# Kernel optimization log

Measured on AMD Instinct MI355X. Metric: run time of the kernel, lower is better.

The kernel has to match this reference:

```python
import jax, jax.numpy as jnp
import numpy as np

D_MODEL, N_HEADS, D_VALUE = 512, 8, 64
D_HEAD = D_MODEL // N_HEADS


def setup_inputs() -> dict:
    key = jax.random.key(0)
    ks = jax.random.split(key, 5)
    B, T = 2, 2048
    x = jax.random.normal(ks[0], (B, T, D_MODEL), dtype=jnp.float32)
    # torch nn.Linear convention: W has shape [out_features, in_features]
    scale = 0.02
    W_q = jax.random.normal(ks[1], (N_HEADS * D_HEAD, D_MODEL), dtype=jnp.float32) * scale
    W_k = jax.random.normal(ks[2], (N_HEADS * D_HEAD, D_MODEL), dtype=jnp.float32) * scale
    W_v = jax.random.normal(ks[3], (N_HEADS * D_VALUE, D_MODEL), dtype=jnp.float32) * scale
    W_out = jax.random.normal(ks[4], (D_MODEL, N_HEADS * D_VALUE), dtype=jnp.float32) * scale
    return {"x": x, "W_q": W_q, "W_k": W_k, "W_v": W_v, "W_out": W_out}


def _elu_feature_map(t):
    # phi(t) = elu(t) + 1
    return jax.nn.elu(t) + 1.0


def reference(x, W_q, W_k, W_v, W_out):
    B, T, D = x.shape
    H, dh, dv = N_HEADS, D_HEAD, D_VALUE
    # projections (Linear without bias: x @ W.T)
    Q = _elu_feature_map((x @ W_q.T).reshape(B, T, H, dh)).transpose(0, 2, 1, 3)  # [B,H,T,dh]
    K = _elu_feature_map((x @ W_k.T).reshape(B, T, H, dh)).transpose(0, 2, 1, 3)  # [B,H,T,dh]
    V = (x @ W_v.T).reshape(B, T, H, dv).transpose(0, 2, 1, 3)                    # [B,H,T,dv]
    # causal linear attention via cumulative outer-product state
    KV = jnp.einsum('bhti,bhtj->bhtij', K, V)       # [B,H,T,dh,dv]
    S = jnp.cumsum(KV, axis=2)                      # running state
    z = jnp.cumsum(K, axis=2)                       # running normalizer
    num = jnp.einsum('bhti,bhtij->bhtj', Q, S)      # [B,H,T,dv]
    den = jnp.maximum(jnp.einsum('bhti,bhti->bht', Q, z), 1e-6)[..., None]
    out = (num / den).transpose(0, 2, 1, 3).reshape(B, T, H * dv)
    return out @ W_out.T
```

## Files before the change

kernel.cpp:

```cpp
#include <hip/hip_runtime.h>
#include <hip/hip_bf16.h>

#define T_SEQ 2048
#define BATCH 2
#define DMODEL 512
#define NHEAD 8
#define DHEAD 64
#define DVAL 64
#define BH 16
#define CHUNK 64
#define NCHUNK 32
#define MROWS 4096

typedef __bf16 bf16;
typedef __bf16 bf16x8 __attribute__((ext_vector_type(8)));
typedef __bf16 bf16x4 __attribute__((ext_vector_type(4)));
typedef float f32x4 __attribute__((ext_vector_type(4)));

__device__ inline void gload_lds16(const bf16* g, bf16* l) {
  __builtin_amdgcn_global_load_lds((const __attribute__((address_space(1))) void*)g,
                                   (__attribute__((address_space(3))) void*)l, 16, 0, 0);
}

__device__ inline int sw_t(int row, int g) {
  return ((g ^ (row & 7) ^ (row >> 3)) << 3);
}

__global__ __launch_bounds__(256) void k_convert(const float* __restrict__ x,
                          const float* __restrict__ wq,
                          const float* __restrict__ wk,
                          const float* __restrict__ wv,
                          const float* __restrict__ wo,
                          bf16* __restrict__ x_bf,
                          bf16* __restrict__ wqkv_bf,
                          bf16* __restrict__ wo_bf) {
  const int W = DMODEL * DMODEL;
  int i = blockIdx.x * 256 + threadIdx.x;
  {
    f32x4 v = ((const f32x4*)x)[i];
    bf16x4 o; o[0] = (bf16)v[0]; o[1] = (bf16)v[1]; o[2] = (bf16)v[2]; o[3] = (bf16)v[3];
    *(bf16x4*)(x_bf + (size_t)i * 4) = o;
  }
  if (i < W / 4) {
    f32x4 a = ((const f32x4*)wq)[i];
    f32x4 b = ((const f32x4*)wk)[i];
    f32x4 c = ((const f32x4*)wv)[i];
    f32x4 d = ((const f32x4*)wo)[i];
    bf16x4 oa, ob, oc, od;
#pragma unroll
    for (int u = 0; u < 4; u++) { oa[u] = (bf16)a[u]; ob[u] = (bf16)b[u]; oc[u] = (bf16)c[u]; od[u] = (bf16)d[u]; }
    *(bf16x4*)(wqkv_bf + (size_t)i * 4) = oa;
    *(bf16x4*)(wqkv_bf + W + (size_t)i * 4) = ob;
    *(bf16x4*)(wqkv_bf + 2 * W + (size_t)i * 4) = oc;
    *(bf16x4*)(wo_bf + (size_t)i * 4) = od;
  }
}

template <int EPI>
__global__ __launch_bounds__(256) void k_gemm(const bf16* __restrict__ A,
                                              const bf16* __restrict__ B,
                                              bf16* __restrict__ Q,
                                              bf16* __restrict__ K,
                                              bf16* __restrict__ V,
                                              float* __restrict__ out) {
  __shared__ bf16 As[128 * 64];
  __shared__ bf16 Bs[128 * 64];
  const int tid = threadIdx.x;
  const int wv = tid >> 6, lane = tid & 63;
  const int c = lane & 15, quad = lane >> 4;
  const int m_tile = blockIdx.x * 128, n_tile = blockIdx.y * 128;
  const int r8 = lane >> 3, gp = lane & 7;
  const bf16* Abase = A + (size_t)m_tile * DMODEL;
  const bf16* Bbase = B + (size_t)n_tile * DMODEL;
  const int wm = (wv >> 1) * 64, wn = (wv & 1) * 64;

  f32x4 acc[4][4] = {};

  for (int k0 = 0; k0 < DMODEL; k0 += 64) {
    if (k0) __syncthreads();
#pragma unroll
    for (int r = 0; r < 4; r++) {
      int t = wv * 4 + r;
      const bf16* ga = Abase + (size_t)(t * 8 + r8) * DMODEL + k0 + ((gp ^ r8) << 3);
      const bf16* gb = Bbase + (size_t)(t * 8 + r8) * DMODEL + k0 + ((gp ^ r8) << 3);
      gload_lds16(ga, As + t * 8 * 64);
      gload_lds16(gb, Bs + t * 8 * 64);
    }
    __syncthreads();
#pragma unroll
    for (int ks = 0; ks < 2; ks++) {
      bf16x8 af[4], bfr[4];
#pragma unroll
      for (int i = 0; i < 4; i++)
        af[i] = *(const bf16x8*)(As + (wm + i * 16 + c) * 64 + (((ks * 4 + quad) ^ (c & 7)) << 3));
#pragma unroll
      for (int j = 0; j < 4; j++)
        bfr[j] = *(const bf16x8*)(Bs + (wn + j * 16 + c) * 64 + (((ks * 4 + quad) ^ (c & 7)) << 3));
#pragma unroll
      for (int i = 0; i < 4; i++)
#pragma unroll
        for (int j = 0; j < 4; j++)
          acc[i][j] = __builtin_amdgcn_mfma_f32_16x16x32_bf16(af[i], bfr[j], acc[i][j], 0, 0, 0);
    }
  }

#pragma unroll
  for (int i = 0; i < 4; i++) {
#pragma unroll
    for (int j = 0; j < 4; j++) {
      int n = n_tile + wn + j * 16 + c;
#pragma unroll
      for (int r = 0; r < 4; r++) {
        int m = m_tile + wm + i * 16 + quad * 4 + r;
        float v = acc[i][j][r];
        if (EPI == 0) {
          if (n < 1024) v = (v > 0.f) ? (v + 1.f) : __expf(v);
          bf16 o = (bf16)v;
          if (n < 512)       Q[(size_t)m * 512 + n] = o;
          else if (n < 1024) K[(size_t)m * 512 + (n - 512)] = o;
          else               V[(size_t)m * 512 + (n - 1024)] = o;
        } else {
          out[(size_t)m * DMODEL + n] = v;
        }
      }
    }
  }
}

__global__ __launch_bounds__(256) void k_state(const bf16* __restrict__ K,
                                               const bf16* __restrict__ V,
                                               bf16* __restrict__ KVs,
                                               float* __restrict__ zsum) {
  __shared__ bf16 Kt[4096];
  __shared__ bf16 Vt[4096];
  int chunk = blockIdx.x, bh = blockIdx.y;
  int b = bh >> 3, h = bh & 7;
  int tid = threadIdx.x, lane = tid & 63, wv = tid >> 6;
  int rowbase = b * T_SEQ + chunk * CHUNK;

#pragma unroll
  for (int p = 0; p < 2; p++) {
    int r = p * 32 + (tid >> 3);
    int j0 = (tid & 7) * 8;
    bf16x8 kk = *(const bf16x8*)(K + (size_t)(rowbase + r) * 512 + h * 64 + j0);
    bf16x8 vvv = *(const bf16x8*)(V + (size_t)(rowbase + r) * 512 + h * 64 + j0);
#pragma unroll
    for (int u = 0; u < 8; u++) {
      int row = j0 + u;
      Kt[row * 64 + sw_t(row, r >> 3) + (r & 7)] = kk[u];
      Vt[row * 64 + sw_t(row, r >> 3) + (r & 7)] = vvv[u];
    }
  }
  __syncthreads();

  int c = lane & 15, quad = lane >> 4;
  f32x4 acc[4] = {};
#pragma unroll
  for (int ks = 0; ks < 2; ks++) {
    int ar = wv * 16 + c;
    bf16x8 a = *(const bf16x8*)(Vt + ar * 64 + sw_t(ar, ks * 4 + quad));
#pragma unroll
    for (int f = 0; f < 4; f++) {
      int br = f * 16 + c;
      bf16x8 bb = *(const bf16x8*)(Kt + br * 64 + sw_t(br, ks * 4 + quad));
      acc[f] = __builtin_amdgcn_mfma_f32_16x16x32_bf16(a, bb, acc[f], 0, 0, 0);
    }
  }
  bf16* op = KVs + ((size_t)(bh * NCHUNK + chunk) << 12);
#pragma unroll
  for (int f = 0; f < 4; f++)
#pragma unroll
    for (int r = 0; r < 4; r++)
      op[(wv * 16 + quad * 4 + r) * 64 + f * 16 + c] = (bf16)acc[f][r];

  if (tid < 64) {
    float s = 0.f;
#pragma unroll
    for (int g = 0; g < 8; g++) {
      bf16x8 kr = *(const bf16x8*)(Kt + tid * 64 + sw_t(tid, g));
#pragma unroll
      for (int u = 0; u < 8; u++) s += (float)kr[u];
    }
    zsum[(size_t)(bh * NCHUNK + chunk) * 64 + tid] = s;
  }
}

__global__ __launch_bounds__(256) void k_attn(const bf16* __restrict__ Q,
                                              const bf16* __restrict__ K,
                                              const bf16* __restrict__ V,
                                              const bf16* __restrict__ KVs,
                                              const float* __restrict__ zsum,
                                              bf16* __restrict__ O) {
  __shared__ bf16 Qs[4096];
  __shared__ bf16 Ks[4096];
  __shared__ bf16 Vt[4096];
  __shared__ bf16 As[4096];
  __shared__ bf16 Spre[4096];
  __shared__ float zp4[4][64];
  __shared__ float zpre[64], rsum[64], den[64];

  int chunk = blockIdx.x, bh = blockIdx.y;
  int b = bh >> 3, h = bh & 7;
  int tid = threadIdx.x, lane = tid & 63, wv = tid >> 6;
  int c = lane & 15, quad = lane >> 4;
  int rowbase = b * T_SEQ + chunk * CHUNK;

#pragma unroll
  for (int p = 0; p < 2; p++) {
    int rbase = p * 32 + wv * 8;
    int r8 = lane >> 3, gp = lane & 7;
    const bf16* gq = Q + (size_t)(rowbase + rbase + r8) * 512 + h * 64 + ((gp ^ r8) << 3);
    const bf16* gk = K + (size_t)(rowbase + rbase + r8) * 512 + h * 64 + ((gp ^ r8) << 3);
    gload_lds16(gq, Qs + rbase * 64);
    gload_lds16(gk, Ks + rbase * 64);
  }

#pragma unroll
  for (int p = 0; p < 2; p++) {
    int r = p * 32 + (tid >> 3);
    int j0 = (tid & 7) * 8;
    bf16x8 vvv = *(const bf16x8*)(V + (size_t)(rowbase + r) * 512 + h * 64 + j0);
#pragma unroll
    for (int u = 0; u < 8; u++) {
      int row = j0 + u;
      Vt[row * 64 + sw_t(row, r >> 3) + (r & 7)] = vvv[u];
    }
  }

  {
    float accp[16];
#pragma unroll
    for (int u = 0; u < 16; u++) accp[u] = 0.f;
    const bf16* base = KVs + ((size_t)(bh * NCHUNK) << 12) + tid * 16;
    for (int cc = 0; cc < chunk; cc++) {
      const bf16* pp = base + ((size_t)cc << 12);
      bf16x8 a0 = *(const bf16x8*)pp;
      bf16x8 a1 = *(const bf16x8*)(pp + 8);
#pragma unroll
      for (int u = 0; u < 8; u++) { accp[u] += (float)a0[u]; accp[8 + u] += (float)a1[u]; }
    }
    int j = tid >> 2, i0 = (tid & 3) * 16;
#pragma unroll
    for (int u = 0; u < 16; u++) {
      int i = i0 + u;
      Spre[j * 64 + sw_t(j, i >> 3) + (i & 7)] = (bf16)accp[u];
    }
  }

  {
    int i = tid & 63, qq = tid >> 6;
    float s = 0.f;
    for (int cc = qq; cc < chunk; cc += 4)
      s += zsum[(size_t)(bh * NCHUNK + cc) * 64 + i];
    zp4[qq][i] = s;
  }
  __syncthreads();
  if (tid < 64) zpre[tid] = zp4[0][tid] + zp4[1][tid] + zp4[2][tid] + zp4[3][tid];

  f32x4 sacc[4] = {};
#pragma unroll
  for (int ks = 0; ks < 2; ks++) {
    int ar = 16 * wv + c;
    bf16x8 a = *(const bf16x8*)(Qs + ar * 64 + (((ks * 4 + quad) ^ (c & 7)) << 3));
#pragma unroll
    for (int j = 0; j < 4; j++) {
      int br = 16 * j + c;
      bf16x8 bb = *(const bf16x8*)(Ks + br * 64 + (((ks * 4 + quad) ^ (c & 7)) << 3));
      sacc[j] = __builtin_amdgcn_mfma_f32_16x16x32_bf16(a, bb, sacc[j], 0, 0, 0);
    }
  }

  float rs[4] = {0.f, 0.f, 0.f, 0.f};
#pragma unroll
  for (int j = 0; j < 4; j++) {
#pragma unroll
    for (int r = 0; r < 4; r++) {
      int t = 16 * wv + quad * 4 + r, s = 16 * j + c;
      float v = (s <= t) ? sacc[j][r] : 0.f;
      rs[r] += v;
      As[t * 64 + sw_t(t, s >> 3) + (s & 7)] = (bf16)v;
    }
  }
#pragma unroll
  for (int r = 0; r < 4; r++) {
    float v = rs[r];
    v += __shfl_xor(v, 1); v += __shfl_xor(v, 2);
    v += __shfl_xor(v, 4); v += __shfl_xor(v, 8);
    if (c == 0) rsum[16 * wv + quad * 4 + r] = v;
  }
  __syncthreads();

  if (tid < 64) {
    float s = rsum[tid];
    int t7 = tid & 7;
#pragma unroll
    for (int kg = 0; kg < 8; kg++) {
      bf16x8 qv = *(const bf16x8*)(Qs + tid * 64 + ((kg ^ t7) << 3));
#pragma unroll
      for (int u = 0; u < 8; u++) s += (float)qv[u] * zpre[kg * 8 + u];
    }
    den[tid] = fmaxf(s, 1e-6f);
  }

  f32x4 oacc[4] = {};
#pragma unroll
  for (int ks = 0; ks < 2; ks++) {
    int ar = 16 * wv + c;
    bf16x8 aq = *(const bf16x8*)(Qs + ar * 64 + (((ks * 4 + quad) ^ (c & 7)) << 3));
    bf16x8 aa = *(const bf16x8*)(As + ar * 64 + sw_t(ar, ks * 4 + quad));
#pragma unroll
    for (int j = 0; j < 4; j++) {
      int br = 16 * j + c;
      bf16x8 bs = *(const bf16x8*)(Spre + br * 64 + sw_t(br, ks * 4 + quad));
      bf16x8 bv = *(const bf16x8*)(Vt + br * 64 + sw_t(br, ks * 4 + quad));
      oacc[j] = __builtin_amdgcn_mfma_f32_16x16x32_bf16(aq, bs, oacc[j], 0, 0, 0);
      oacc[j] = __builtin_amdgcn_mfma_f32_16x16x32_bf16(aa, bv, oacc[j], 0, 0, 0);
    }
  }
  __syncthreads();
#pragma unroll
  for (int r = 0; r < 4; r++) {
    int t = 16 * wv + quad * 4 + r;
    float rd = 1.f / den[t];
#pragma unroll
    for (int j = 0; j < 4; j++)
      O[(size_t)(rowbase + t) * 512 + h * 64 + 16 * j + c] = (bf16)(oacc[j][r] * rd);
  }
}

extern "C" void kernel_launch(void* const* d_in, const int* in_sizes, int n_in,
                              void* d_out, int out_size, void* d_ws, size_t ws_size,
                              hipStream_t stream) {
  const float* x  = (const float*)d_in[0];
  const float* wq = (const float*)d_in[1];
  const float* wk = (const float*)d_in[2];
  const float* wv = (const float*)d_in[3];
  const float* wo = (const float*)d_in[4];
  float* out = (float*)d_out;

  char* p = (char*)d_ws;
  bf16* x_bf   = (bf16*)p; p += (size_t)MROWS * DMODEL * 2;
  bf16* wqkv_b = (bf16*)p; p += (size_t)3 * DMODEL * DMODEL * 2;
  bf16* wo_b   = (bf16*)p; p += (size_t)DMODEL * DMODEL * 2;
  bf16* Qb     = (bf16*)p; p += (size_t)MROWS * 512 * 2;
  bf16* Kb     = (bf16*)p; p += (size_t)MROWS * 512 * 2;
  bf16* Vb     = (bf16*)p; p += (size_t)MROWS * 512 * 2;
  bf16* Ob     = (bf16*)p; p += (size_t)MROWS * 512 * 2;
  bf16* KVs    = (bf16*)p; p += (size_t)BH * NCHUNK * DHEAD * DVAL * 2;
  float* zs    = (float*)p; p += (size_t)BH * NCHUNK * DHEAD * 4;

  k_convert<<<2048, 256, 0, stream>>>(x, wq, wk, wv, wo, x_bf, wqkv_b, wo_b);
  k_gemm<0><<<dim3(MROWS / 128, (3 * DMODEL) / 128), 256, 0, stream>>>(
      x_bf, wqkv_b, Qb, Kb, Vb, nullptr);
  k_state<<<dim3(NCHUNK, BH), 256, 0, stream>>>(Kb, Vb, KVs, zs);
  k_attn<<<dim3(NCHUNK, BH), 256, 0, stream>>>(Qb, Kb, Vb, KVs, zs, Ob);
  k_gemm<1><<<dim3(MROWS / 128, DMODEL / 128), 256, 0, stream>>>(
      Ob, wo_b, nullptr, nullptr, nullptr, out);
}
```

Measured before the change: 119.9 us.

## Fuse chunk-state and attention kernels via cooperative grid sync; stage GEMM epilogues through LDS

Merges the per-chunk KV state kernel into the attention kernel and joins them with a cooperative grid-wide sync, so K and V are loaded once and one launch is removed. The GEMM epilogues now stage tiles through shared memory so the Q/K/V and output writes go out as coalesced 16-byte vectors, and the attention output is written the same way. The per-chunk state is stored in a fragment-native layout, and the prefix-sum read path is changed to match. A grid sync over 512 blocks needs every block to be resident at once. It also adds sync latency and more shared memory per block.

```diff
diff --git a/kernel.cpp b/kernel.cpp
--- a/kernel.cpp
+++ b/kernel.cpp
@@ -1,5 +1,6 @@
 #include <hip/hip_runtime.h>
 #include <hip/hip_bf16.h>
+#include <hip/hip_cooperative_groups.h>
 
 #define T_SEQ 2048
 #define BATCH 2
@@ -63,16 +64,17 @@
                                               bf16* __restrict__ K,
                                               bf16* __restrict__ V,
                                               float* __restrict__ out) {
-  __shared__ bf16 As[128 * 64];
-  __shared__ bf16 Bs[128 * 64];
+  __shared__ bf16 sh[16896];
+  bf16* As = sh;
+  bf16* Bs = sh + 8192;
   const int tid = threadIdx.x;
-  const int wv = tid >> 6, lane = tid & 63;
+  const int wvi = tid >> 6, lane = tid & 63;
   const int c = lane & 15, quad = lane >> 4;
   const int m_tile = blockIdx.x * 128, n_tile = blockIdx.y * 128;
   const int r8 = lane >> 3, gp = lane & 7;
   const bf16* Abase = A + (size_t)m_tile * DMODEL;
   const bf16* Bbase = B + (size_t)n_tile * DMODEL;
-  const int wm = (wv >> 1) * 64, wn = (wv & 1) * 64;
+  const int wm = (wvi >> 1) * 64, wn = (wvi & 1) * 64;
 
   f32x4 acc[4][4] = {};
 
@@ -80,7 +82,7 @@
     if (k0) __syncthreads();
 #pragma unroll
     for (int r = 0; r < 4; r++) {
-      int t = wv * 4 + r;
+      int t = wvi * 4 + r;
       const bf16* ga = Abase + (size_t)(t * 8 + r8) * DMODEL + k0 + ((gp ^ r8) << 3);
       const bf16* gb = Bbase + (size_t)(t * 8 + r8) * DMODEL + k0 + ((gp ^ r8) << 3);
       gload_lds16(ga, As + t * 8 * 64);
@@ -104,110 +106,81 @@
     }
   }
 
-#pragma unroll
-  for (int i = 0; i < 4; i++) {
-#pragma unroll
-    for (int j = 0; j < 4; j++) {
-      int n = n_tile + wn + j * 16 + c;
-#pragma unroll
-      for (int r = 0; r < 4; r++) {
-        int m = m_tile + wm + i * 16 + quad * 4 + r;
-        float v = acc[i][j][r];
-        if (EPI == 0) {
-          if (n < 1024) v = (v > 0.f) ? (v + 1.f) : __expf(v);
-          bf16 o = (bf16)v;
-          if (n < 512)       Q[(size_t)m * 512 + n] = o;
-          else if (n < 1024) K[(size_t)m * 512 + (n - 512)] = o;
-          else               V[(size_t)m * 512 + (n - 1024)] = o;
-        } else {
-          out[(size_t)m * DMODEL + n] = v;
+  if (EPI == 0) {
+    const bool is_qk = (n_tile < 1024);
+    __syncthreads();
+#pragma unroll
+    for (int i = 0; i < 4; i++)
+#pragma unroll
+      for (int j = 0; j < 4; j++)
+#pragma unroll
+        for (int r = 0; r < 4; r++) {
+          int row = wm + i * 16 + quad * 4 + r;
+          int col = wn + j * 16 + c;
+          float v = acc[i][j][r];
+          if (is_qk) v = (v > 0.f) ? (v + 1.f) : __expf(v);
+          sh[row * 132 + col] = (bf16)v;
         }
+    __syncthreads();
+    bf16* dst = (n_tile < 512) ? Q : ((n_tile < 1024) ? K : V);
+    int nb = n_tile & 511;
+#pragma unroll
+    for (int q = 0; q < 8; q++) {
+      int row = q * 16 + (tid >> 4);
+      int col0 = (tid & 15) * 8;
+      bf16x8 v8 = *(const bf16x8*)(sh + row * 132 + col0);
+      *(bf16x8*)(dst + (size_t)(m_tile + row) * 512 + nb + col0) = v8;
+    }
+  } else {
+    float* shf = (float*)sh;
+#pragma unroll
+    for (int p = 0; p < 2; p++) {
+      __syncthreads();
+      if ((wvi >> 1) == p) {
+#pragma unroll
+        for (int i = 0; i < 4; i++)
+#pragma unroll
+          for (int j = 0; j < 4; j++)
+#pragma unroll
+            for (int r = 0; r < 4; r++)
+              shf[(i * 16 + quad * 4 + r) * 132 + wn + j * 16 + c] = acc[i][j][r];
       }
-    }
-  }
-}
-
-__global__ __launch_bounds__(256) void k_state(const bf16* __restrict__ K,
-                                               const bf16* __restrict__ V,
-                                               bf16* __restrict__ KVs,
-                                               float* __restrict__ zsum) {
-  __shared__ bf16 Kt[4096];
-  __shared__ bf16 Vt[4096];
+      __syncthreads();
+      int row = tid >> 2, col0 = (tid & 3) * 32;
+#pragma unroll
+      for (int q4 = 0; q4 < 8; q4++) {
+        f32x4 v4 = *(const f32x4*)(shf + row * 132 + col0 + q4 * 4);
+        *(f32x4*)(out + (size_t)(m_tile + p * 64 + row) * 512 + n_tile + col0 + q4 * 4) = v4;
+      }
+    }
+  }
+}
+
+__global__ __launch_bounds__(256) void k_attn_fused(const bf16* __restrict__ Q,
+                                                    const bf16* __restrict__ K,
+                                                    const bf16* __restrict__ V,
+                                                    bf16* __restrict__ KVs,
+                                                    float* __restrict__ zsum,
+                                                    bf16* __restrict__ O) {
+  __shared__ bf16 SH[24576];
+  bf16* Qs   = SH;
+  bf16* Ks   = SH + 4096;
+  bf16* Vt   = SH + 8192;
+  bf16* Kt   = SH + 12288;
+  bf16* Asm  = SH + 16384;
+  bf16* Spre = SH + 20480;
+  __shared__ float zp4[4][64];
+  __shared__ float zpre[64], rsum[64], den[64];
+
   int chunk = blockIdx.x, bh = blockIdx.y;
   int b = bh >> 3, h = bh & 7;
-  int tid = threadIdx.x, lane = tid & 63, wv = tid >> 6;
-  int rowbase = b * T_SEQ + chunk * CHUNK;
-
-#pragma unroll
-  for (int p = 0; p < 2; p++) {
-    int r = p * 32 + (tid >> 3);
-    int j0 = (tid & 7) * 8;
-    bf16x8 kk = *(const bf16x8*)(K + (size_t)(rowbase + r) * 512 + h * 64 + j0);
-    bf16x8 vvv = *(const bf16x8*)(V + (size_t)(rowbase + r) * 512 + h * 64 + j0);
-#pragma unroll
-    for (int u = 0; u < 8; u++) {
-      int row = j0 + u;
-      Kt[row * 64 + sw_t(row, r >> 3) + (r & 7)] = kk[u];
-      Vt[row * 64 + sw_t(row, r >> 3) + (r & 7)] = vvv[u];
-    }
-  }
-  __syncthreads();
-
-  int c = lane & 15, quad = lane >> 4;
-  f32x4 acc[4] = {};
-#pragma unroll
-  for (int ks = 0; ks < 2; ks++) {
-    int ar = wv * 16 + c;
-    bf16x8 a = *(const bf16x8*)(Vt + ar * 64 + sw_t(ar, ks * 4 + quad));
-#pragma unroll
-    for (int f = 0; f < 4; f++) {
-      int br = f * 16 + c;
-      bf16x8 bb = *(const bf16x8*)(Kt + br * 64 + sw_t(br, ks * 4 + quad));
-      acc[f] = __builtin_amdgcn_mfma_f32_16x16x32_bf16(a, bb, acc[f], 0, 0, 0);
-    }
-  }
-  bf16* op = KVs + ((size_t)(bh * NCHUNK + chunk) << 12);
-#pragma unroll
-  for (int f = 0; f < 4; f++)
-#pragma unroll
-    for (int r = 0; r < 4; r++)
-      op[(wv * 16 + quad * 4 + r) * 64 + f * 16 + c] = (bf16)acc[f][r];
-
-  if (tid < 64) {
-    float s = 0.f;
-#pragma unroll
-    for (int g = 0; g < 8; g++) {
-      bf16x8 kr = *(const bf16x8*)(Kt + tid * 64 + sw_t(tid, g));
-#pragma unroll
-      for (int u = 0; u < 8; u++) s += (float)kr[u];
-    }
-    zsum[(size_t)(bh * NCHUNK + chunk) * 64 + tid] = s;
-  }
-}
-
-__global__ __launch_bounds__(256) void k_attn(const bf16* __restrict__ Q,
-                                              const bf16* __restrict__ K,
-                                              const bf16* __restrict__ V,
-                                              const bf16* __restrict__ KVs,
-                                              const float* __restrict__ zsum,
-                                              bf16* __restrict__ O) {
-  __shared__ bf16 Qs[4096];
-  __shared__ bf16 Ks[4096];
-  __shared__ bf16 Vt[4096];
-  __shared__ bf16 As[4096];
-  __shared__ bf16 Spre[4096];
-  __shared__ float zp4[4][64];
-  __shared__ float zpre[64], rsum[64], den[64];
-
-  int chunk = blockIdx.x, bh = blockIdx.y;
-  int b = bh >> 3, h = bh & 7;
-  int tid = threadIdx.x, lane = tid & 63, wv = tid >> 6;
+  int tid = threadIdx.x, lane = tid & 63, wvi = tid >> 6;
   int c = lane & 15, quad = lane >> 4;
   int rowbase = b * T_SEQ + chunk * CHUNK;
 
 #pragma unroll
   for (int p = 0; p < 2; p++) {
-    int rbase = p * 32 + wv * 8;
+    int rbase = p * 32 + wvi * 8;
     int r8 = lane >> 3, gp = lane & 7;
     const bf16* gq = Q + (size_t)(rowbase + rbase + r8) * 512 + h * 64 + ((gp ^ r8) << 3);
     const bf16* gk = K + (size_t)(rowbase + rbase + r8) * 512 + h * 64 + ((gp ^ r8) << 3);
@@ -219,13 +192,52 @@
   for (int p = 0; p < 2; p++) {
     int r = p * 32 + (tid >> 3);
     int j0 = (tid & 7) * 8;
+    bf16x8 kk  = *(const bf16x8*)(K + (size_t)(rowbase + r) * 512 + h * 64 + j0);
     bf16x8 vvv = *(const bf16x8*)(V + (size_t)(rowbase + r) * 512 + h * 64 + j0);
 #pragma unroll
     for (int u = 0; u < 8; u++) {
       int row = j0 + u;
+      Kt[row * 64 + sw_t(row, r >> 3) + (r & 7)] = kk[u];
       Vt[row * 64 + sw_t(row, r >> 3) + (r & 7)] = vvv[u];
     }
   }
+  __syncthreads();
+
+  {
+    f32x4 acc[4] = {};
+#pragma unroll
+    for (int ks = 0; ks < 2; ks++) {
+      int ar = wvi * 16 + c;
+      bf16x8 a = *(const bf16x8*)(Vt + ar * 64 + sw_t(ar, ks * 4 + quad));
+#pragma unroll
+      for (int f = 0; f < 4; f++) {
+        int br = f * 16 + c;
+        bf16x8 bb = *(const bf16x8*)(Kt + br * 64 + sw_t(br, ks * 4 + quad));
+        acc[f] = __builtin_amdgcn_mfma_f32_16x16x32_bf16(a, bb, acc[f], 0, 0, 0);
+      }
+    }
+    bf16* op = KVs + ((size_t)(bh * NCHUNK + chunk) << 12);
+    bf16x8 lo, hi;
+#pragma unroll
+    for (int u = 0; u < 8; u++) {
+      lo[u] = (bf16)acc[u >> 2][u & 3];
+      hi[u] = (bf16)acc[2 + (u >> 2)][u & 3];
+    }
+    *(bf16x8*)(op + tid * 16) = lo;
+    *(bf16x8*)(op + tid * 16 + 8) = hi;
+  }
+  if (tid < 64) {
+    float s = 0.f;
+#pragma unroll
+    for (int g = 0; g < 8; g++) {
+      bf16x8 kr = *(const bf16x8*)(Kt + tid * 64 + sw_t(tid, g));
+#pragma unroll
+      for (int u = 0; u < 8; u++) s += (float)kr[u];
+    }
+    zsum[(size_t)(bh * NCHUNK + chunk) * 64 + tid] = s;
+  }
+  __threadfence();
+  cooperative_groups::this_grid().sync();
 
   {
     float accp[16];
@@ -239,14 +251,13 @@
 #pragma unroll
       for (int u = 0; u < 8; u++) { accp[u] += (float)a0[u]; accp[8 + u] += (float)a1[u]; }
     }
-    int j = tid >> 2, i0 = (tid & 3) * 16;
-#pragma unroll
-    for (int u = 0; u < 16; u++) {
-      int i = i0 + u;
-      Spre[j * 64 + sw_t(j, i >> 3) + (i & 7)] = (bf16)accp[u];
-    }
-  }
-
+#pragma unroll
+    for (int s = 0; s < 16; s++) {
+      int rowp = wvi * 16 + quad * 4 + (s & 3);
+      int colp = (s >> 2) * 16 + c;
+      Spre[rowp * 64 + sw_t(rowp, colp >> 3) + (colp & 7)] = (bf16)accp[s];
+    }
+  }
   {
     int i = tid & 63, qq = tid >> 6;
     float s = 0.f;
@@ -260,7 +271,7 @@
   f32x4 sacc[4] = {};
 #pragma unroll
   for (int ks = 0; ks < 2; ks++) {
-    int ar = 16 * wv + c;
+    int ar = 16 * wvi + c;
     bf16x8 a = *(const bf16x8*)(Qs + ar * 64 + (((ks * 4 + quad) ^ (c & 7)) << 3));
 #pragma unroll
     for (int j = 0; j < 4; j++) {
@@ -275,10 +286,10 @@
   for (int j = 0; j < 4; j++) {
 #pragma unroll
     for (int r = 0; r < 4; r++) {
-      int t = 16 * wv + quad * 4 + r, s = 16 * j + c;
+      int t = 16 * wvi + quad * 4 + r, s = 16 * j + c;
       float v = (s <= t) ? sacc[j][r] : 0.f;
       rs[r] += v;
-      As[t * 64 + sw_t(t, s >> 3) + (s & 7)] = (bf16)v;
+      Asm[t * 64 + sw_t(t, s >> 3) + (s & 7)] = (bf16)v;
     }
   }
 #pragma unroll
@@ -286,7 +297,7 @@
     float v = rs[r];
     v += __shfl_xor(v, 1); v += __shfl_xor(v, 2);
     v += __shfl_xor(v, 4); v += __shfl_xor(v, 8);
-    if (c == 0) rsum[16 * wv + quad * 4 + r] = v;
+    if (c == 0) rsum[16 * wvi + quad * 4 + r] = v;
   }
   __syncthreads();
 
@@ -305,9 +316,9 @@
   f32x4 oacc[4] = {};
 #pragma unroll
   for (int ks = 0; ks < 2; ks++) {
-    int ar = 16 * wv + c;
+    int ar = 16 * wvi + c;
     bf16x8 aq = *(const bf16x8*)(Qs + ar * 64 + (((ks * 4 + quad) ^ (c & 7)) << 3));
-    bf16x8 aa = *(const bf16x8*)(As + ar * 64 + sw_t(ar, ks * 4 + quad));
+    bf16x8 aa = *(const bf16x8*)(Asm + ar * 64 + sw_t(ar, ks * 4 + quad));
 #pragma unroll
     for (int j = 0; j < 4; j++) {
       int br = 16 * j + c;
@@ -318,13 +329,24 @@
     }
   }
   __syncthreads();
-#pragma unroll
-  for (int r = 0; r < 4; r++) {
-    int t = 16 * wv + quad * 4 + r;
-    float rd = 1.f / den[t];
-#pragma unroll
-    for (int j = 0; j < 4; j++)
-      O[(size_t)(rowbase + t) * 512 + h * 64 + 16 * j + c] = (bf16)(oacc[j][r] * rd);
+
+  {
+    bf16* shr = SH;
+#pragma unroll
+    for (int r = 0; r < 4; r++) {
+      int t = 16 * wvi + quad * 4 + r;
+      float rd = 1.f / den[t];
+#pragma unroll
+      for (int j = 0; j < 4; j++)
+        shr[t * 76 + 16 * j + c] = (bf16)(oacc[j][r] * rd);
+    }
+    __syncthreads();
+    int row = tid >> 2, col0 = (tid & 3) * 16;
+    bf16x8 v0 = *(const bf16x8*)(shr + row * 76 + col0);
+    bf16x8 v1 = *(const bf16x8*)(shr + row * 76 + col0 + 8);
+    bf16* od = O + (size_t)(rowbase + row) * 512 + h * 64 + col0;
+    *(bf16x8*)od = v0;
+    *(bf16x8*)(od + 8) = v1;
   }
 }
 
@@ -352,8 +374,15 @@
   k_convert<<<2048, 256, 0, stream>>>(x, wq, wk, wv, wo, x_bf, wqkv_b, wo_b);
   k_gemm<0><<<dim3(MROWS / 128, (3 * DMODEL) / 128), 256, 0, stream>>>(
       x_bf, wqkv_b, Qb, Kb, Vb, nullptr);
-  k_state<<<dim3(NCHUNK, BH), 256, 0, stream>>>(Kb, Vb, KVs, zs);
-  k_attn<<<dim3(NCHUNK, BH), 256, 0, stream>>>(Qb, Kb, Vb, KVs, zs, Ob);
+
+  {
+    const bf16* aQ = Qb; const bf16* aK = Kb; const bf16* aV = Vb;
+    bf16* aKV = KVs; float* aZ = zs; bf16* aO = Ob;
+    void* args[6] = {(void*)&aQ, (void*)&aK, (void*)&aV, (void*)&aKV, (void*)&aZ, (void*)&aO};
+    hipLaunchCooperativeKernel((const void*)k_attn_fused, dim3(NCHUNK, BH), dim3(256),
+                               args, 0, stream);
+  }
+
   k_gemm<1><<<dim3(MROWS / 128, DMODEL / 128), 256, 0, stream>>>(
       Ob, wo_b, nullptr, nullptr, nullptr, out);
 }
```

Measured after the change: 251.6 us. 110% more time.
